# Performance work log

Hardware: AMD Instinct MI355X
Metric: run time of the kernel (lower is better)

## Reference

```python
import jax, jax.numpy as jnp
import numpy as np

B, S, H, D = 8, 16, 32, 64
HID = H * D
PAST = 4096


def setup_inputs() -> dict:
    key = jax.random.key(0)
    ks = jax.random.split(key, 7)
    sc = 0.02
    return {
        "hidden_states": jax.random.normal(ks[0], (B, S, HID), jnp.float32),
        "past_k": jax.random.normal(ks[1], (B, H, PAST, D), jnp.float32),
        "past_v": jax.random.normal(ks[2], (B, H, PAST, D), jnp.float32),
        "wq": jax.random.normal(ks[3], (HID, HID), jnp.float32) * sc,
        "wk": jax.random.normal(ks[4], (HID, HID), jnp.float32) * sc,
        "wv": jax.random.normal(ks[5], (HID, HID), jnp.float32) * sc,
        "wo": jax.random.normal(ks[6], (HID, HID), jnp.float32) * sc,
    }


def reference(hidden_states, past_k, past_v, wq, wk, wv, wo):
    b, s, _ = hidden_states.shape
    # QKV projections (torch Linear: x @ W.T), split into heads -> [B,H,S,D]
    q = (hidden_states @ wq.T).reshape(b, s, H, D).transpose(0, 2, 1, 3)
    k = (hidden_states @ wk.T).reshape(b, s, H, D).transpose(0, 2, 1, 3)
    v = (hidden_states @ wv.T).reshape(b, s, H, D).transpose(0, 2, 1, 3)
    # KV-cache concat: [B,H,past+S,D]
    k = jnp.concatenate([past_k, k], axis=2)
    v = jnp.concatenate([past_v, v], axis=2)
    scale = 1.0 / jnp.sqrt(jnp.asarray(D, hidden_states.dtype))
    # scores [B,H,S,T]
    scores = jnp.einsum("bhsd,bhtd->bhst", q, k) * scale
    probs = jax.nn.softmax(scores, axis=-1)
    out = jnp.einsum("bhst,bhtd->bhsd", probs, v)
    out = out.transpose(0, 2, 1, 3).reshape(b, s, HID)
    return out @ wo.T
```

## Files before the change

### kernel.cpp

```cpp
#include <hip/hip_runtime.h>
#include <hip/hip_bf16.h>
#include <stdint.h>

#define HID 2048
#define NH  32
#define HD  64
#define NB  8
#define NS  16
#define PAST 4096

#define QSCALE 0.18033688011112042591f

typedef __attribute__((ext_vector_type(8))) short short8;
typedef __attribute__((ext_vector_type(4))) short short4v;
typedef __attribute__((ext_vector_type(4))) float f32x4;

#define MFMA(a, b, c) __builtin_amdgcn_mfma_f32_16x16x32_bf16((a), (b), (c), 0, 0, 0)

#define PART_STRIDE 1088
#define NSPLIT 4
#define VSLAB  8704

static __device__ __forceinline__ short f2bf(float f) {
    __hip_bfloat16 h = __float2bfloat16(f);
    return *reinterpret_cast<short*>(&h);
}

static __device__ __forceinline__ short8 pack8(float4 a, float4 b) {
    short8 r;
    r[0] = f2bf(a.x); r[1] = f2bf(a.y); r[2] = f2bf(a.z); r[3] = f2bf(a.w);
    r[4] = f2bf(b.x); r[5] = f2bf(b.y); r[6] = f2bf(b.z); r[7] = f2bf(b.w);
    return r;
}

static __device__ __forceinline__ short4v pack4(float4 a) {
    short4v r;
    r[0] = f2bf(a.x); r[1] = f2bf(a.y); r[2] = f2bf(a.z); r[3] = f2bf(a.w);
    return r;
}

static __device__ __forceinline__ short8 pack8s(float4 a, float4 b, float s) {
    short8 r;
    r[0] = f2bf(a.x * s); r[1] = f2bf(a.y * s); r[2] = f2bf(a.z * s); r[3] = f2bf(a.w * s);
    r[4] = f2bf(b.x * s); r[5] = f2bf(b.y * s); r[6] = f2bf(b.z * s); r[7] = f2bf(b.w * s);
    return r;
}

__global__ __launch_bounds__(256) void cvt_kernel(const float* __restrict__ in,
                                                  short* __restrict__ out) {
    int i = (blockIdx.x * 256 + threadIdx.x) * 4;
    float4 v = *reinterpret_cast<const float4*>(in + i);
    short4v o;
    o[0] = f2bf(v.x); o[1] = f2bf(v.y); o[2] = f2bf(v.z); o[3] = f2bf(v.w);
    *reinterpret_cast<short4v*>(out + i) = o;
}

__global__ __launch_bounds__(128) void proj_kernel(
        const short* __restrict__ X,
        const float* __restrict__ W0, const float* __restrict__ W1,
        const float* __restrict__ W2,
        float* __restrict__ Y0, float* __restrict__ Y1, float* __restrict__ Y2) {
    int mat   = blockIdx.x >> 9;
    int rest  = blockIdx.x & 511;
    int strip = rest >> 2, ks = rest & 3;
    int nbase = strip * 16;
    int k0    = ks * 512;
    const float* W = (mat == 0) ? W0 : (mat == 1) ? W1 : W2;
    float*       Y = (mat == 0) ? Y0 : (mat == 1) ? Y1 : Y2;

    int lane = threadIdx.x & 63;
    int wave = threadIdx.x >> 6;
    int lr = lane & 15, g = lane >> 4;

    f32x4 acc0 = {0.f, 0.f, 0.f, 0.f};
    f32x4 acc1 = {0.f, 0.f, 0.f, 0.f};
    f32x4 acc2 = {0.f, 0.f, 0.f, 0.f};
    f32x4 acc3 = {0.f, 0.f, 0.f, 0.f};

    const short* xr = X + (size_t)(wave * 64 + lr) * HID + g * 8 + k0;
    const float* wr = W + (size_t)(nbase + lr) * HID + g * 8 + k0;

    #pragma unroll 4
    for (int kc = 0; kc < 512; kc += 32) {
        float4 w0 = *reinterpret_cast<const float4*>(wr + kc);
        float4 w1 = *reinterpret_cast<const float4*>(wr + kc + 4);
        short8 bb = pack8(w0, w1);
        short8 a0 = *reinterpret_cast<const short8*>(xr + kc);
        short8 a1 = *reinterpret_cast<const short8*>(xr + (size_t)16 * HID + kc);
        short8 a2 = *reinterpret_cast<const short8*>(xr + (size_t)32 * HID + kc);
        short8 a3 = *reinterpret_cast<const short8*>(xr + (size_t)48 * HID + kc);
        acc0 = MFMA(a0, bb, acc0);
        acc1 = MFMA(a1, bb, acc1);
        acc2 = MFMA(a2, bb, acc2);
        acc3 = MFMA(a3, bb, acc3);
    }
    #define STACC(accv, f) do { \
        atomicAdd(&Y[(size_t)(wave * 64 + (f) * 16 + (g << 2) + 0) * HID + nbase + lr], accv[0]); \
        atomicAdd(&Y[(size_t)(wave * 64 + (f) * 16 + (g << 2) + 1) * HID + nbase + lr], accv[1]); \
        atomicAdd(&Y[(size_t)(wave * 64 + (f) * 16 + (g << 2) + 2) * HID + nbase + lr], accv[2]); \
        atomicAdd(&Y[(size_t)(wave * 64 + (f) * 16 + (g << 2) + 3) * HID + nbase + lr], accv[3]); \
    } while (0)
    STACC(acc0, 0); STACC(acc1, 1); STACC(acc2, 2); STACC(acc3, 3);
    #undef STACC
}

__global__ __launch_bounds__(256, 4) void attn_kernel(
        const float* __restrict__ q,
        const float* __restrict__ knew, const float* __restrict__ vnew,
        const float* __restrict__ pastK, const float* __restrict__ pastV,
        float* __restrict__ parts) {
    __shared__ __align__(16) unsigned char lds_raw[4 * VSLAB];
    __shared__ float s_m[4][16];
    __shared__ float s_l[4][16];

    int bid = blockIdx.x;
    int bh = bid >> 2, split = bid & 3;
    int b = bh >> 5, h = bh & 31;
    int wave = threadIdx.x >> 6, lane = threadIdx.x & 63;
    int lq = lane & 15, g = lane >> 4;

    unsigned short* vsl = (unsigned short*)(lds_raw + wave * VSLAB);

    const float* qp = q + (size_t)(b * NS + lq) * HID + h * HD + g * 8;
    short8 qf0, qf1;
    {
        float4 a0 = *reinterpret_cast<const float4*>(qp);
        float4 a1 = *reinterpret_cast<const float4*>(qp + 4);
        float4 a2 = *reinterpret_cast<const float4*>(qp + 32);
        float4 a3 = *reinterpret_cast<const float4*>(qp + 36);
        qf0 = pack8s(a0, a1, QSCALE);
        qf1 = pack8s(a2, a3, QSCALE);
    }

    f32x4 o0 = {0.f, 0.f, 0.f, 0.f};
    f32x4 o1 = {0.f, 0.f, 0.f, 0.f};
    f32x4 o2 = {0.f, 0.f, 0.f, 0.f};
    f32x4 o3 = {0.f, 0.f, 0.f, 0.f};
    float m = -__builtin_inff(), lsum = 0.0f;

    const float* kbase = pastK + (size_t)bh * PAST * HD + (size_t)(split * 1024 + wave * 256) * HD;
    const float* vbase = pastV + (size_t)bh * PAST * HD + (size_t)(split * 1024 + wave * 256) * HD;

    #define KLD(s2i) \
        const float* kr##s2i = kbase + (size_t)(pb + (s2i) * 16 + lq) * HD + (g << 3); \
        float4 ka##s2i = *reinterpret_cast<const float4*>(kr##s2i); \
        float4 kb##s2i = *reinterpret_cast<const float4*>(kr##s2i + 4); \
        float4 kc##s2i = *reinterpret_cast<const float4*>(kr##s2i + 32); \
        float4 kd##s2i = *reinterpret_cast<const float4*>(kr##s2i + 36);

    #define KMM(scv, s2i) do { \
        short8 af0 = pack8(ka##s2i, kb##s2i); \
        short8 af1 = pack8(kc##s2i, kd##s2i); \
        f32x4 sv = {0.f, 0.f, 0.f, 0.f}; \
        sv = MFMA(af0, qf0, sv); \
        sv = MFMA(af1, qf1, sv); \
        scv = sv; \
    } while (0)

    #define VLD(I) float4 vld##I = *reinterpret_cast<const float4*>(vt + (I) * 256 + lane * 4);
    #define VST(I) *reinterpret_cast<short4v*>(vsl + (4 * (I) + g) * 68 + lq * 4) = pack4(vld##I);

    #define LV(p, d) ((short)vsl[(p) * 68 + (d)])
    #define VFR(dst, kfo, dcol) do { \
        dst[0] = LV((kfo) + (g << 2) + 0, (dcol)); \
        dst[1] = LV((kfo) + (g << 2) + 1, (dcol)); \
        dst[2] = LV((kfo) + (g << 2) + 2, (dcol)); \
        dst[3] = LV((kfo) + (g << 2) + 3, (dcol)); \
        dst[4] = LV((kfo) + 16 + (g << 2) + 0, (dcol)); \
        dst[5] = LV((kfo) + 16 + (g << 2) + 1, (dcol)); \
        dst[6] = LV((kfo) + 16 + (g << 2) + 2, (dcol)); \
        dst[7] = LV((kfo) + 16 + (g << 2) + 3, (dcol)); \
    } while (0)

    #define PEXP(dst, idx, sv, r) do { \
        float e = exp2f(sv[r] - mn); rsum += e; dst[idx] = f2bf(e); \
    } while (0)

    #pragma unroll 1
    for (int t = 0; t < 4; ++t) {
        int pb = t * 64;
        const float* vt = vbase + (size_t)pb * HD;

        KLD(0) KLD(1) KLD(2) KLD(3)
        VLD(0) VLD(1) VLD(2) VLD(3) VLD(4) VLD(5) VLD(6) VLD(7)

        f32x4 sc0, sc1, sc2, sc3;
        KMM(sc0, 0); KMM(sc1, 1); KMM(sc2, 2); KMM(sc3, 3);

        VLD(8) VLD(9) VLD(10) VLD(11) VLD(12) VLD(13) VLD(14) VLD(15)

        float tmax = fmaxf(
            fmaxf(fmaxf(fmaxf(sc0[0], sc0[1]), fmaxf(sc0[2], sc0[3])),
                  fmaxf(fmaxf(sc1[0], sc1[1]), fmaxf(sc1[2], sc1[3]))),
            fmaxf(fmaxf(fmaxf(sc2[0], sc2[1]), fmaxf(sc2[2], sc2[3])),
                  fmaxf(fmaxf(sc3[0], sc3[1]), fmaxf(sc3[2], sc3[3]))));
        tmax = fmaxf(tmax, __shfl_xor(tmax, 16));
        tmax = fmaxf(tmax, __shfl_xor(tmax, 32));
        float mn = fmaxf(m, tmax);
        float alpha = exp2f(m - mn);
        float rsum = 0.f;
        short8 pf0, pf1;
        PEXP(pf0, 0, sc0, 0); PEXP(pf0, 1, sc0, 1); PEXP(pf0, 2, sc0, 2); PEXP(pf0, 3, sc0, 3);
        PEXP(pf0, 4, sc1, 0); PEXP(pf0, 5, sc1, 1); PEXP(pf0, 6, sc1, 2); PEXP(pf0, 7, sc1, 3);
        PEXP(pf1, 0, sc2, 0); PEXP(pf1, 1, sc2, 1); PEXP(pf1, 2, sc2, 2); PEXP(pf1, 3, sc2, 3);
        PEXP(pf1, 4, sc3, 0); PEXP(pf1, 5, sc3, 1); PEXP(pf1, 6, sc3, 2); PEXP(pf1, 7, sc3, 3);
        rsum += __shfl_xor(rsum, 16);
        rsum += __shfl_xor(rsum, 32);
        lsum = lsum * alpha + rsum;
        m = mn;
        o0 *= alpha; o1 *= alpha; o2 *= alpha; o3 *= alpha;

        VST(0); VST(1); VST(2); VST(3); VST(4); VST(5); VST(6); VST(7);

        {
            short8 vfa;
            VFR(vfa, 0, lq);       o0 = MFMA(vfa, pf0, o0);
            VFR(vfa, 0, 16 + lq);  o1 = MFMA(vfa, pf0, o1);
            VFR(vfa, 0, 32 + lq);  o2 = MFMA(vfa, pf0, o2);
            VFR(vfa, 0, 48 + lq);  o3 = MFMA(vfa, pf0, o3);
        }

        VST(8); VST(9); VST(10); VST(11); VST(12); VST(13); VST(14); VST(15);

        {
            short8 vfb;
            VFR(vfb, 32, lq);       o0 = MFMA(vfb, pf1, o0);
            VFR(vfb, 32, 16 + lq);  o1 = MFMA(vfb, pf1, o1);
            VFR(vfb, 32, 32 + lq);  o2 = MFMA(vfb, pf1, o2);
            VFR(vfb, 32, 48 + lq);  o3 = MFMA(vfb, pf1, o3);
        }
    }

    if (split == 0 && wave == 0) {
        const float* kr = knew + (size_t)(b * NS + lq) * HID + h * HD + g * 8;
        float4 ka = *reinterpret_cast<const float4*>(kr);
        float4 kb2 = *reinterpret_cast<const float4*>(kr + 4);
        float4 kc2 = *reinterpret_cast<const float4*>(kr + 32);
        float4 kd2 = *reinterpret_cast<const float4*>(kr + 36);
        short8 af0 = pack8(ka, kb2);
        short8 af1 = pack8(kc2, kd2);
        f32x4 sv = {0.f, 0.f, 0.f, 0.f};
        sv = MFMA(af0, qf0, sv);
        sv = MFMA(af1, qf1, sv);

        float tmax = fmaxf(fmaxf(sv[0], sv[1]), fmaxf(sv[2], sv[3]));
        tmax = fmaxf(tmax, __shfl_xor(tmax, 16));
        tmax = fmaxf(tmax, __shfl_xor(tmax, 32));
        float mn = fmaxf(m, tmax);
        float alpha = exp2f(m - mn);
        float e0 = exp2f(sv[0] - mn);
        float e1 = exp2f(sv[1] - mn);
        float e2 = exp2f(sv[2] - mn);
        float e3 = exp2f(sv[3] - mn);
        float rsum = e0 + e1 + e2 + e3;
        rsum += __shfl_xor(rsum, 16);
        rsum += __shfl_xor(rsum, 32);
        lsum = lsum * alpha + rsum;
        m = mn;
        o0 *= alpha; o1 *= alpha; o2 *= alpha; o3 *= alpha;

        short8 pfT;
        pfT[0] = f2bf(e0); pfT[1] = f2bf(e1); pfT[2] = f2bf(e2); pfT[3] = f2bf(e3);
        pfT[4] = 0; pfT[5] = 0; pfT[6] = 0; pfT[7] = 0;

        const float* vt2 = vnew + (size_t)(b * NS) * HID + h * HD;
        #define LOADVT(dst, dcol) do { \
            dst[0] = f2bf(vt2[(size_t)((g << 2) + 0) * HID + (dcol)]); \
            dst[1] = f2bf(vt2[(size_t)((g << 2) + 1) * HID + (dcol)]); \
            dst[2] = f2bf(vt2[(size_t)((g << 2) + 2) * HID + (dcol)]); \
            dst[3] = f2bf(vt2[(size_t)((g << 2) + 3) * HID + (dcol)]); \
            dst[4] = 0; dst[5] = 0; dst[6] = 0; dst[7] = 0; \
        } while (0)
        short8 vv0, vv1, vv2, vv3;
        LOADVT(vv0, lq); LOADVT(vv1, 16 + lq); LOADVT(vv2, 32 + lq); LOADVT(vv3, 48 + lq);
        #undef LOADVT
        o0 = MFMA(vv0, pfT, o0);
        o1 = MFMA(vv1, pfT, o1);
        o2 = MFMA(vv2, pfT, o2);
        o3 = MFMA(vv3, pfT, o3);
    }

    __syncthreads();
    float* so_w = (float*)(lds_raw + wave * VSLAB);
    #define STO(ov, dt) do { \
        so_w[lq * 64 + (dt) * 16 + (g << 2) + 0] = ov[0]; \
        so_w[lq * 64 + (dt) * 16 + (g << 2) + 1] = ov[1]; \
        so_w[lq * 64 + (dt) * 16 + (g << 2) + 2] = ov[2]; \
        so_w[lq * 64 + (dt) * 16 + (g << 2) + 3] = ov[3]; \
    } while (0)
    STO(o0, 0); STO(o1, 1); STO(o2, 2); STO(o3, 3);
    #undef STO
    if (g == 0) { s_m[wave][lq] = m; s_l[wave][lq] = lsum; }
    __syncthreads();

    if (wave == 0) {
        float M = fmaxf(fmaxf(s_m[0][lq], s_m[1][lq]), fmaxf(s_m[2][lq], s_m[3][lq]));
        float aw0 = exp2f(s_m[0][lq] - M);
        float aw1 = exp2f(s_m[1][lq] - M);
        float aw2 = exp2f(s_m[2][lq] - M);
        float aw3 = exp2f(s_m[3][lq] - M);
        float L = aw0 * s_l[0][lq] + aw1 * s_l[1][lq] + aw2 * s_l[2][lq] + aw3 * s_l[3][lq];
        const float* so0 = (const float*)(lds_raw + 0 * VSLAB);
        const float* so1 = (const float*)(lds_raw + 1 * VSLAB);
        const float* so2 = (const float*)(lds_raw + 2 * VSLAB);
        const float* so3 = (const float*)(lds_raw + 3 * VSLAB);
        float* pbase = parts + (size_t)bid * PART_STRIDE;
        if (g == 0) { pbase[lq] = M; pbase[16 + lq] = L; }
        for (int dd = 0; dd < 16; ++dd) {
            int di = g * 16 + dd;
            float v = aw0 * so0[lq * 64 + di] + aw1 * so1[lq * 64 + di] +
                      aw2 * so2[lq * 64 + di] + aw3 * so3[lq * 64 + di];
            pbase[32 + lq * 64 + di] = v;
        }
    }
}

__global__ __launch_bounds__(256) void merge_kernel(const float* __restrict__ parts,
                                                    short* __restrict__ attnb) {
    int bh = blockIdx.x;
    int tid = threadIdx.x;
    int qi = tid >> 4, ds = (tid & 15) * 4;
    const float* p0 = parts + (size_t)(bh * NSPLIT) * PART_STRIDE;
    const float* p1 = p0 + PART_STRIDE;
    const float* p2 = p1 + PART_STRIDE;
    const float* p3 = p2 + PART_STRIDE;
    float m0 = p0[qi], m1 = p1[qi], m2 = p2[qi], m3 = p3[qi];
    float M = fmaxf(fmaxf(m0, m1), fmaxf(m2, m3));
    float a0 = exp2f(m0 - M), a1 = exp2f(m1 - M), a2 = exp2f(m2 - M), a3 = exp2f(m3 - M);
    float inv = 1.0f / (a0 * p0[16 + qi] + a1 * p1[16 + qi] +
                        a2 * p2[16 + qi] + a3 * p3[16 + qi]);
    int b = bh >> 5, h = bh & 31;
    int base = 32 + qi * 64 + ds;
    float v0 = (a0 * p0[base + 0] + a1 * p1[base + 0] + a2 * p2[base + 0] + a3 * p3[base + 0]) * inv;
    float v1 = (a0 * p0[base + 1] + a1 * p1[base + 1] + a2 * p2[base + 1] + a3 * p3[base + 1]) * inv;
    float v2 = (a0 * p0[base + 2] + a1 * p1[base + 2] + a2 * p2[base + 2] + a3 * p3[base + 2]) * inv;
    float v3 = (a0 * p0[base + 3] + a1 * p1[base + 3] + a2 * p2[base + 3] + a3 * p3[base + 3]) * inv;
    short4v o;
    o[0] = f2bf(v0); o[1] = f2bf(v1); o[2] = f2bf(v2); o[3] = f2bf(v3);
    *reinterpret_cast<short4v*>(attnb + (size_t)(b * NS + qi) * HID + h * HD + ds) = o;
}

extern "C" void kernel_launch(void* const* d_in, const int* in_sizes, int n_in,
                              void* d_out, int out_size, void* d_ws, size_t ws_size,
                              hipStream_t stream) {
    const float* hs     = (const float*)d_in[0];
    const float* past_k = (const float*)d_in[1];
    const float* past_v = (const float*)d_in[2];
    const float* wq     = (const float*)d_in[3];
    const float* wk     = (const float*)d_in[4];
    const float* wv     = (const float*)d_in[5];
    const float* wo     = (const float*)d_in[6];
    float* out = (float*)d_out;

    float* qb = (float*)d_ws;
    float* kn = qb + 128 * 2048;
    float* vn = kn + 128 * 2048;
    short* hsb   = (short*)(vn + 128 * 2048);
    short* attnb = hsb + 128 * 2048;
    float* parts = (float*)(attnb + 128 * 2048);

    hipMemsetAsync(qb, 0, (size_t)3 * 128 * 2048 * sizeof(float), stream);
    hipMemsetAsync(out, 0, (size_t)128 * 2048 * sizeof(float), stream);

    cvt_kernel<<<256, 256, 0, stream>>>(hs, hsb);
    proj_kernel<<<1536, 128, 0, stream>>>(hsb, wq, wk, wv, qb, kn, vn);
    attn_kernel<<<256 * NSPLIT, 256, 0, stream>>>(qb, kn, vn, past_k, past_v, parts);
    merge_kernel<<<256, 256, 0, stream>>>(parts, attnb);
    proj_kernel<<<512, 128, 0, stream>>>(attnb, wo, wo, wo, out, out, out);
}
```

Baseline: 210.2 us.

## Double-buffer V tiles into LDS via async global_load_lds across the block

Restructures the attention split loop. Previously each wave privately processed 256 keys, loading V into registers, converting it to bf16 and storing it to a per-wave LDS slab. Now the whole block walks 16 tiles of 64 keys, with each wave taking 16 keys per tile. The fp32 V tiles are staged into a double-buffered LDS array with async global_load_lds, and each tile ends in a block-wide barrier. The goal is to overlap V loads with compute and drop the register round trip for V. The cost is that each MFMA now uses only half its K dimension, since half the operand is zero padding. It also adds a __syncthreads per tile and does strided fp32 LDS reads with per-element bf16 conversion.

```diff
diff --git a/kernel.cpp b/kernel.cpp
--- a/kernel.cpp
+++ b/kernel.cpp
@@ -19,23 +19,24 @@
 
 #define PART_STRIDE 1088
 #define NSPLIT 4
-#define VSLAB  8704
+#define NTILES 16
 
 static __device__ __forceinline__ short f2bf(float f) {
     __hip_bfloat16 h = __float2bfloat16(f);
     return *reinterpret_cast<short*>(&h);
+}
+
+static __device__ __forceinline__ void gload_lds16(const float* g, float* l) {
+    __builtin_amdgcn_global_load_lds(
+        (const __attribute__((address_space(1))) void*)(g),
+        (__attribute__((address_space(3))) void*)(l),
+        16, 0, 0);
 }
 
 static __device__ __forceinline__ short8 pack8(float4 a, float4 b) {
     short8 r;
     r[0] = f2bf(a.x); r[1] = f2bf(a.y); r[2] = f2bf(a.z); r[3] = f2bf(a.w);
     r[4] = f2bf(b.x); r[5] = f2bf(b.y); r[6] = f2bf(b.z); r[7] = f2bf(b.w);
-    return r;
-}
-
-static __device__ __forceinline__ short4v pack4(float4 a) {
-    short4v r;
-    r[0] = f2bf(a.x); r[1] = f2bf(a.y); r[2] = f2bf(a.z); r[3] = f2bf(a.w);
     return r;
 }
 
@@ -109,7 +110,7 @@
         const float* __restrict__ knew, const float* __restrict__ vnew,
         const float* __restrict__ pastK, const float* __restrict__ pastV,
         float* __restrict__ parts) {
-    __shared__ __align__(16) unsigned char lds_raw[4 * VSLAB];
+    __shared__ __align__(16) float lds_v[2][64 * 64];
     __shared__ float s_m[4][16];
     __shared__ float s_l[4][16];
 
@@ -118,8 +119,6 @@
     int b = bh >> 5, h = bh & 31;
     int wave = threadIdx.x >> 6, lane = threadIdx.x & 63;
     int lq = lane & 15, g = lane >> 4;
-
-    unsigned short* vsl = (unsigned short*)(lds_raw + wave * VSLAB);
 
     const float* qp = q + (size_t)(b * NS + lq) * HID + h * HD + g * 8;
     short8 qf0, qf1;
@@ -138,107 +137,32 @@
     f32x4 o3 = {0.f, 0.f, 0.f, 0.f};
     float m = -__builtin_inff(), lsum = 0.0f;
 
-    const float* kbase = pastK + (size_t)bh * PAST * HD + (size_t)(split * 1024 + wave * 256) * HD;
-    const float* vbase = pastV + (size_t)bh * PAST * HD + (size_t)(split * 1024 + wave * 256) * HD;
-
-    #define KLD(s2i) \
-        const float* kr##s2i = kbase + (size_t)(pb + (s2i) * 16 + lq) * HD + (g << 3); \
-        float4 ka##s2i = *reinterpret_cast<const float4*>(kr##s2i); \
-        float4 kb##s2i = *reinterpret_cast<const float4*>(kr##s2i + 4); \
-        float4 kc##s2i = *reinterpret_cast<const float4*>(kr##s2i + 32); \
-        float4 kd##s2i = *reinterpret_cast<const float4*>(kr##s2i + 36);
-
-    #define KMM(scv, s2i) do { \
-        short8 af0 = pack8(ka##s2i, kb##s2i); \
-        short8 af1 = pack8(kc##s2i, kd##s2i); \
-        f32x4 sv = {0.f, 0.f, 0.f, 0.f}; \
-        sv = MFMA(af0, qf0, sv); \
-        sv = MFMA(af1, qf1, sv); \
-        scv = sv; \
+    const float* ksplit = pastK + (size_t)bh * PAST * HD + (size_t)split * 1024 * HD;
+    const float* vsplit = pastV + (size_t)bh * PAST * HD + (size_t)split * 1024 * HD;
+
+    #define STAGE(tt, dstf) do { \
+        const float* gsrc_ = vsplit + (size_t)(tt) * 64 * HD; \
+        gload_lds16(gsrc_ + (wave * 4 + 0) * 256 + lane * 4, (dstf) + (wave * 4 + 0) * 256); \
+        gload_lds16(gsrc_ + (wave * 4 + 1) * 256 + lane * 4, (dstf) + (wave * 4 + 1) * 256); \
+        gload_lds16(gsrc_ + (wave * 4 + 2) * 256 + lane * 4, (dstf) + (wave * 4 + 2) * 256); \
+        gload_lds16(gsrc_ + (wave * 4 + 3) * 256 + lane * 4, (dstf) + (wave * 4 + 3) * 256); \
     } while (0)
 
-    #define VLD(I) float4 vld##I = *reinterpret_cast<const float4*>(vt + (I) * 256 + lane * 4);
-    #define VST(I) *reinterpret_cast<short4v*>(vsl + (4 * (I) + g) * 68 + lq * 4) = pack4(vld##I);
-
-    #define LV(p, d) ((short)vsl[(p) * 68 + (d)])
-    #define VFR(dst, kfo, dcol) do { \
-        dst[0] = LV((kfo) + (g << 2) + 0, (dcol)); \
-        dst[1] = LV((kfo) + (g << 2) + 1, (dcol)); \
-        dst[2] = LV((kfo) + (g << 2) + 2, (dcol)); \
-        dst[3] = LV((kfo) + (g << 2) + 3, (dcol)); \
-        dst[4] = LV((kfo) + 16 + (g << 2) + 0, (dcol)); \
-        dst[5] = LV((kfo) + 16 + (g << 2) + 1, (dcol)); \
-        dst[6] = LV((kfo) + 16 + (g << 2) + 2, (dcol)); \
-        dst[7] = LV((kfo) + 16 + (g << 2) + 3, (dcol)); \
-    } while (0)
-
-    #define PEXP(dst, idx, sv, r) do { \
-        float e = exp2f(sv[r] - mn); rsum += e; dst[idx] = f2bf(e); \
-    } while (0)
-
+    STAGE(0, lds_v[0]);
+    __syncthreads();
+
+    int cur = 0;
     #pragma unroll 1
-    for (int t = 0; t < 4; ++t) {
-        int pb = t * 64;
-        const float* vt = vbase + (size_t)pb * HD;
-
-        KLD(0) KLD(1) KLD(2) KLD(3)
-        VLD(0) VLD(1) VLD(2) VLD(3) VLD(4) VLD(5) VLD(6) VLD(7)
-
-        f32x4 sc0, sc1, sc2, sc3;
-        KMM(sc0, 0); KMM(sc1, 1); KMM(sc2, 2); KMM(sc3, 3);
-
-        VLD(8) VLD(9) VLD(10) VLD(11) VLD(12) VLD(13) VLD(14) VLD(15)
-
-        float tmax = fmaxf(
-            fmaxf(fmaxf(fmaxf(sc0[0], sc0[1]), fmaxf(sc0[2], sc0[3])),
-                  fmaxf(fmaxf(sc1[0], sc1[1]), fmaxf(sc1[2], sc1[3]))),
-            fmaxf(fmaxf(fmaxf(sc2[0], sc2[1]), fmaxf(sc2[2], sc2[3])),
-                  fmaxf(fmaxf(sc3[0], sc3[1]), fmaxf(sc3[2], sc3[3]))));
-        tmax = fmaxf(tmax, __shfl_xor(tmax, 16));
-        tmax = fmaxf(tmax, __shfl_xor(tmax, 32));
-        float mn = fmaxf(m, tmax);
-        float alpha = exp2f(m - mn);
-        float rsum = 0.f;
-        short8 pf0, pf1;
-        PEXP(pf0, 0, sc0, 0); PEXP(pf0, 1, sc0, 1); PEXP(pf0, 2, sc0, 2); PEXP(pf0, 3, sc0, 3);
-        PEXP(pf0, 4, sc1, 0); PEXP(pf0, 5, sc1, 1); PEXP(pf0, 6, sc1, 2); PEXP(pf0, 7, sc1, 3);
-        PEXP(pf1, 0, sc2, 0); PEXP(pf1, 1, sc2, 1); PEXP(pf1, 2, sc2, 2); PEXP(pf1, 3, sc2, 3);
-        PEXP(pf1, 4, sc3, 0); PEXP(pf1, 5, sc3, 1); PEXP(pf1, 6, sc3, 2); PEXP(pf1, 7, sc3, 3);
-        rsum += __shfl_xor(rsum, 16);
-        rsum += __shfl_xor(rsum, 32);
-        lsum = lsum * alpha + rsum;
-        m = mn;
-        o0 *= alpha; o1 *= alpha; o2 *= alpha; o3 *= alpha;
-
-        VST(0); VST(1); VST(2); VST(3); VST(4); VST(5); VST(6); VST(7);
-
-        {
-            short8 vfa;
-            VFR(vfa, 0, lq);       o0 = MFMA(vfa, pf0, o0);
-            VFR(vfa, 0, 16 + lq);  o1 = MFMA(vfa, pf0, o1);
-            VFR(vfa, 0, 32 + lq);  o2 = MFMA(vfa, pf0, o2);
-            VFR(vfa, 0, 48 + lq);  o3 = MFMA(vfa, pf0, o3);
-        }
-
-        VST(8); VST(9); VST(10); VST(11); VST(12); VST(13); VST(14); VST(15);
-
-        {
-            short8 vfb;
-            VFR(vfb, 32, lq);       o0 = MFMA(vfb, pf1, o0);
-            VFR(vfb, 32, 16 + lq);  o1 = MFMA(vfb, pf1, o1);
-            VFR(vfb, 32, 32 + lq);  o2 = MFMA(vfb, pf1, o2);
-            VFR(vfb, 32, 48 + lq);  o3 = MFMA(vfb, pf1, o3);
-        }
-    }
-
-    if (split == 0 && wave == 0) {
-        const float* kr = knew + (size_t)(b * NS + lq) * HID + h * HD + g * 8;
+    for (int t = 0; t < NTILES; ++t) {
+        if (t + 1 < NTILES) STAGE(t + 1, lds_v[cur ^ 1]);
+
+        const float* kr = ksplit + (size_t)(t * 64 + wave * 16 + lq) * HD + (g << 3);
         float4 ka = *reinterpret_cast<const float4*>(kr);
-        float4 kb2 = *reinterpret_cast<const float4*>(kr + 4);
-        float4 kc2 = *reinterpret_cast<const float4*>(kr + 32);
-        float4 kd2 = *reinterpret_cast<const float4*>(kr + 36);
-        short8 af0 = pack8(ka, kb2);
-        short8 af1 = pack8(kc2, kd2);
+        float4 kb = *reinterpret_cast<const float4*>(kr + 4);
+        float4 kc = *reinterpret_cast<const float4*>(kr + 32);
+        float4 kd = *reinterpret_cast<const float4*>(kr + 36);
+        short8 af0 = pack8(ka, kb);
+        short8 af1 = pack8(kc, kd);
         f32x4 sv = {0.f, 0.f, 0.f, 0.f};
         sv = MFMA(af0, qf0, sv);
         sv = MFMA(af1, qf1, sv);
@@ -259,6 +183,60 @@
         m = mn;
         o0 *= alpha; o1 *= alpha; o2 *= alpha; o3 *= alpha;
 
+        short8 pf;
+        pf[0] = f2bf(e0); pf[1] = f2bf(e1); pf[2] = f2bf(e2); pf[3] = f2bf(e3);
+        pf[4] = 0; pf[5] = 0; pf[6] = 0; pf[7] = 0;
+
+        const float* vc = lds_v[cur] + (wave * 16 + (g << 2)) * 64;
+        #define VFR(dst, dcol) do { \
+            dst[0] = f2bf(vc[0 * 64 + (dcol)]); \
+            dst[1] = f2bf(vc[1 * 64 + (dcol)]); \
+            dst[2] = f2bf(vc[2 * 64 + (dcol)]); \
+            dst[3] = f2bf(vc[3 * 64 + (dcol)]); \
+            dst[4] = 0; dst[5] = 0; dst[6] = 0; dst[7] = 0; \
+        } while (0)
+        {
+            short8 vf;
+            VFR(vf, lq);       o0 = MFMA(vf, pf, o0);
+            VFR(vf, 16 + lq);  o1 = MFMA(vf, pf, o1);
+            VFR(vf, 32 + lq);  o2 = MFMA(vf, pf, o2);
+            VFR(vf, 48 + lq);  o3 = MFMA(vf, pf, o3);
+        }
+        #undef VFR
+
+        __syncthreads();
+        cur ^= 1;
+    }
+    #undef STAGE
+
+    if (split == 0 && wave == 0) {
+        const float* kr = knew + (size_t)(b * NS + lq) * HID + h * HD + g * 8;
+        float4 ka = *reinterpret_cast<const float4*>(kr);
+        float4 kb2 = *reinterpret_cast<const float4*>(kr + 4);
+        float4 kc2 = *reinterpret_cast<const float4*>(kr + 32);
+        float4 kd2 = *reinterpret_cast<const float4*>(kr + 36);
+        short8 af0 = pack8(ka, kb2);
+        short8 af1 = pack8(kc2, kd2);
+        f32x4 sv = {0.f, 0.f, 0.f, 0.f};
+        sv = MFMA(af0, qf0, sv);
+        sv = MFMA(af1, qf1, sv);
+
+        float tmax = fmaxf(fmaxf(sv[0], sv[1]), fmaxf(sv[2], sv[3]));
+        tmax = fmaxf(tmax, __shfl_xor(tmax, 16));
+        tmax = fmaxf(tmax, __shfl_xor(tmax, 32));
+        float mn = fmaxf(m, tmax);
+        float alpha = exp2f(m - mn);
+        float e0 = exp2f(sv[0] - mn);
+        float e1 = exp2f(sv[1] - mn);
+        float e2 = exp2f(sv[2] - mn);
+        float e3 = exp2f(sv[3] - mn);
+        float rsum = e0 + e1 + e2 + e3;
+        rsum += __shfl_xor(rsum, 16);
+        rsum += __shfl_xor(rsum, 32);
+        lsum = lsum * alpha + rsum;
+        m = mn;
+        o0 *= alpha; o1 *= alpha; o2 *= alpha; o3 *= alpha;
+
         short8 pfT;
         pfT[0] = f2bf(e0); pfT[1] = f2bf(e1); pfT[2] = f2bf(e2); pfT[3] = f2bf(e3);
         pfT[4] = 0; pfT[5] = 0; pfT[6] = 0; pfT[7] = 0;
@@ -280,8 +258,7 @@
         o3 = MFMA(vv3, pfT, o3);
     }
 
-    __syncthreads();
-    float* so_w = (float*)(lds_raw + wave * VSLAB);
+    float* so_w = (float*)lds_v[0] + wave * 1024;
     #define STO(ov, dt) do { \
         so_w[lq * 64 + (dt) * 16 + (g << 2) + 0] = ov[0]; \
         so_w[lq * 64 + (dt) * 16 + (g << 2) + 1] = ov[1]; \
@@ -300,10 +277,10 @@
         float aw2 = exp2f(s_m[2][lq] - M);
         float aw3 = exp2f(s_m[3][lq] - M);
         float L = aw0 * s_l[0][lq] + aw1 * s_l[1][lq] + aw2 * s_l[2][lq] + aw3 * s_l[3][lq];
-        const float* so0 = (const float*)(lds_raw + 0 * VSLAB);
-        const float* so1 = (const float*)(lds_raw + 1 * VSLAB);
-        const float* so2 = (const float*)(lds_raw + 2 * VSLAB);
-        const float* so3 = (const float*)(lds_raw + 3 * VSLAB);
+        const float* so0 = (const float*)lds_v[0] + 0 * 1024;
+        const float* so1 = (const float*)lds_v[0] + 1 * 1024;
+        const float* so2 = (const float*)lds_v[0] + 2 * 1024;
+        const float* so3 = (const float*)lds_v[0] + 3 * 1024;
         float* pbase = parts + (size_t)bid * PART_STRIDE;
         if (g == 0) { pbase[lq] = M; pbase[16 + lq] = L; }
         for (int dd = 0; dd < 16; ++dd) {
```

After: 170.3 us. 1.23x faster.
